# Kernel tuning notes

Measured on AMD Instinct MI355X. Metric: run time of the kernel, lower is better.

## Reference

```python
import jax, jax.numpy as jnp
import numpy as np
from jax import lax

EPS = 1e-5
B, T, I, H = 524288, 6, 4, 20


def batchnorm1d(x, gamma, beta):
    # x: [B, C, L]; training-mode BatchNorm1d over (batch, L) per channel C,
    # biased variance, matching torch's normalization in train().
    mean = jnp.mean(x, axis=(0, 2), keepdims=True)
    var = jnp.mean(jnp.square(x - mean), axis=(0, 2), keepdims=True)
    xhat = (x - mean) * lax.rsqrt(var + EPS)
    return xhat * gamma[None, :, None] + beta[None, :, None]


def lstm_layer(x, W_ih, W_hh, b_ih, b_hh):
    # x: [B, T, in]; torch gate order i, f, g, o; returns h sequence [B, T, H]
    Bsz = x.shape[0]
    Hd = W_hh.shape[1]
    # precompute input contribution for all steps: [B, T, 4H]
    xg = jnp.einsum('bti,gi->btg', x, W_ih) + b_ih + b_hh

    def step(carry, xg_t):
        h, c = carry
        g = xg_t + h @ W_hh.T  # [B, 4H]
        i, f, gg, o = jnp.split(g, 4, axis=-1)
        i = jax.nn.sigmoid(i)
        f = jax.nn.sigmoid(f)
        gg = jnp.tanh(gg)
        o = jax.nn.sigmoid(o)
        c = f * c + i * gg
        h = o * jnp.tanh(c)
        return (h, c), h

    h0 = jnp.zeros((Bsz, Hd), x.dtype)
    c0 = jnp.zeros((Bsz, Hd), x.dtype)
    _, hs = lax.scan(step, (h0, c0), jnp.swapaxes(xg, 0, 1))  # [T, B, H]
    return jnp.swapaxes(hs, 0, 1)


def setup_inputs() -> dict:
    key = jax.random.key(0)
    ks = jax.random.split(key, 12)
    s_ih0 = 1.0 / np.sqrt(H)
    d = {
        'x': jax.random.normal(ks[0], (B, T, I), jnp.float32),
        'gamma': jnp.ones((T,), jnp.float32),
        'beta': jnp.zeros((T,), jnp.float32),
        'W_ih0': jax.random.uniform(ks[1], (4 * H, I), jnp.float32, -s_ih0, s_ih0),
        'W_hh0': jax.random.uniform(ks[2], (4 * H, H), jnp.float32, -s_ih0, s_ih0),
        'b_ih0': jax.random.uniform(ks[3], (4 * H,), jnp.float32, -s_ih0, s_ih0),
        'b_hh0': jax.random.uniform(ks[4], (4 * H,), jnp.float32, -s_ih0, s_ih0),
        'W_ih1': jax.random.uniform(ks[5], (4 * H, H), jnp.float32, -s_ih0, s_ih0),
        'W_hh1': jax.random.uniform(ks[6], (4 * H, H), jnp.float32, -s_ih0, s_ih0),
        'b_ih1': jax.random.uniform(ks[7], (4 * H,), jnp.float32, -s_ih0, s_ih0),
        'b_hh1': jax.random.uniform(ks[8], (4 * H,), jnp.float32, -s_ih0, s_ih0),
        'W_out': jax.random.uniform(ks[9], (1, H), jnp.float32, -s_ih0, s_ih0),
        'b_out': jax.random.uniform(ks[10], (1,), jnp.float32, -s_ih0, s_ih0),
    }
    return d


def reference(x, gamma, beta, W_ih0, W_hh0, b_ih0, b_hh0,
              W_ih1, W_hh1, b_ih1, b_hh1, W_out, b_out):
    # bn over time-channel axis (C = TIME_STEP = 6)
    x = batchnorm1d(x, gamma, beta)                # [B, 6, 4]
    h1 = lstm_layer(x, W_ih0, W_hh0, b_ih0, b_hh0)  # [B, 6, 20]
    h2 = lstm_layer(h1, W_ih1, W_hh1, b_ih1, b_hh1)  # [B, 6, 20]
    r = batchnorm1d(h2, gamma, beta)               # same shared bn module
    out = r[:, -1, :] @ W_out.T + b_out            # [B, 1]
    return out
```

## Files before the change

kernel.cpp:

```cpp
#include <hip/hip_runtime.h>

#define EPS 1e-5f
#define BATCH 524288
#define BLK 256
#define RBLK 256
#define NBLK2 4096
#define NBLKO 2048

typedef float f32x4 __attribute__((ext_vector_type(4)));
typedef __bf16 bf16x8 __attribute__((ext_vector_type(8)));
typedef __bf16 bf16x4 __attribute__((ext_vector_type(4)));

#define AF_A0    0
#define AF_A1K0  5120
#define AF_A1K1  10240
#define AF_TOT   11520
#define OFF_BIAS0 5760
#define OFF_BIAS1 5840
#define OFF_ST    5920
#define OFF_P1    5936
#define OFF_P2    (OFF_P1 + RBLK * 12)

__device__ __forceinline__ float sigm(float x) {
    return __builtin_amdgcn_rcpf(1.0f + __expf(-x));
}
__device__ __forceinline__ float tanh_f(float x) {
    return 1.0f - 2.0f * __builtin_amdgcn_rcpf(1.0f + __expf(2.0f * x));
}
__device__ __forceinline__ float wave_reduce(float v) {
    #pragma unroll
    for (int o = 32; o; o >>= 1) v += __shfl_down(v, o, 64);
    return v;
}

struct HiLo { bf16x8 hi, lo; };
__device__ __forceinline__ HiLo cvt8(f32x4 a, f32x4 b) {
    HiLo r;
    #pragma unroll
    for (int i = 0; i < 4; ++i) {
        float v = a[i];
        __bf16 h = (__bf16)v;
        r.hi[i] = h; r.lo[i] = (__bf16)(v - (float)h);
        float w = b[i];
        __bf16 h2 = (__bf16)w;
        r.hi[4 + i] = h2; r.lo[4 + i] = (__bf16)(w - (float)h2);
    }
    return r;
}
__device__ __forceinline__ bf16x8 zb8() {
    bf16x8 z;
    #pragma unroll
    for (int i = 0; i < 8; ++i) z[i] = (__bf16)0.f;
    return z;
}
#define MFMA16(C_, A_, B_) \
    (C_) = __builtin_amdgcn_mfma_f32_16x16x32_bf16((A_), (B_), (C_), 0, 0, 0)

__global__ __launch_bounds__(BLK) void k_prep(
    const float* __restrict__ Wih0, const float* __restrict__ Whh0,
    const float* __restrict__ bih0, const float* __restrict__ bhh0,
    const float* __restrict__ Wih1, const float* __restrict__ Whh1,
    const float* __restrict__ bih1, const float* __restrict__ bhh1,
    float* __restrict__ ws) {
    const int tid = threadIdx.x;
    unsigned short* af = (unsigned short*)ws;
    for (int idx = tid; idx < AF_TOT; idx += BLK) {
        float w; int s;
        if (idx < AF_A1K0) {
            int e = idx, fid = e >> 9; e &= 511;
            int l = e >> 3, i = e & 7;
            int tm = fid >> 1; s = fid & 1;
            int q = l >> 4, m = l & 15;
            int wrow = (m & 3) * 20 + 4 * tm + (m >> 2);
            int k = 4 * q + (i & 3) + 16 * (i >> 2);
            w = (k < 20) ? Whh0[wrow * 20 + k]
              : (k < 24) ? Wih0[wrow * 4 + (k - 20)] : 0.f;
        } else if (idx < AF_A1K1) {
            int e = idx - AF_A1K0, fid = e >> 9; e &= 511;
            int l = e >> 3, i = e & 7;
            int tm = fid >> 1; s = fid & 1;
            int q = l >> 4, m = l & 15;
            int wrow = (m & 3) * 20 + 4 * tm + (m >> 2);
            int k = 4 * q + (i & 3) + 16 * (i >> 2);
            w = (k < 20) ? Wih1[wrow * 20 + k] : Whh1[wrow * 20 + (k - 20)];
        } else {
            int e = idx - AF_A1K1, fid = e >> 7; e &= 127;
            int l = e >> 2, i = e & 3;
            int tm = fid >> 1; s = fid & 1;
            int q = l >> 4, m = l & 15;
            int wrow = (m & 3) * 20 + 4 * tm + (m >> 2);
            int wcol = 12 + 4 * q + i;
            w = Whh1[wrow * 20 + wcol];
        }
        float fh = (float)(__bf16)w;
        float v = s ? (w - fh) : w;
        __bf16 bv = (__bf16)v;
        af[idx] = __builtin_bit_cast(unsigned short, bv);
    }
    for (int j = tid; j < 80; j += BLK) {
        int tm = j >> 4, q = (j >> 2) & 3, g = j & 3;
        int wrow = g * 20 + 4 * tm + q;
        ws[OFF_BIAS0 + j] = bih0[wrow] + bhh0[wrow];
        ws[OFF_BIAS1 + j] = bih1[wrow] + bhh1[wrow];
    }
}

__global__ __launch_bounds__(BLK) void k_reduce_x(const float* __restrict__ x,
                                                  float* __restrict__ part1) {
    float s[6], q[6];
    #pragma unroll
    for (int t = 0; t < 6; ++t) { s[t] = 0.f; q[t] = 0.f; }
    for (int b = blockIdx.x * BLK + threadIdx.x; b < BATCH; b += RBLK * BLK) {
        const float4* xp = (const float4*)(x + (size_t)b * 24);
        #pragma unroll
        for (int t = 0; t < 6; ++t) {
            float4 v = xp[t];
            s[t] += (v.x + v.y) + (v.z + v.w);
            q[t] += (v.x * v.x + v.y * v.y) + (v.z * v.z + v.w * v.w);
        }
    }
    __shared__ float red[4 * 12];
    int wid = threadIdx.x >> 6, lane = threadIdx.x & 63;
    #pragma unroll
    for (int c = 0; c < 6; ++c) {
        float rs = wave_reduce(s[c]);
        float rq = wave_reduce(q[c]);
        if (lane == 0) { red[wid * 12 + c] = rs; red[wid * 12 + 6 + c] = rq; }
    }
    __syncthreads();
    if (threadIdx.x < 12) {
        float tot = red[threadIdx.x] + red[12 + threadIdx.x] +
                    red[24 + threadIdx.x] + red[36 + threadIdx.x];
        part1[blockIdx.x * 12 + threadIdx.x] = tot;
    }
}

__global__ __launch_bounds__(BLK) void k_stats1(const float* __restrict__ part1,
                                                const float* __restrict__ gamma,
                                                const float* __restrict__ beta,
                                                float* __restrict__ stats) {
    float acc[12];
    #pragma unroll
    for (int c = 0; c < 12; ++c) acc[c] = 0.f;
    for (int p = threadIdx.x; p < RBLK; p += BLK) {
        #pragma unroll
        for (int c = 0; c < 12; ++c) acc[c] += part1[p * 12 + c];
    }
    __shared__ float red[4 * 12];
    __shared__ float tot[12];
    int wid = threadIdx.x >> 6, lane = threadIdx.x & 63;
    #pragma unroll
    for (int c = 0; c < 12; ++c) {
        float r = wave_reduce(acc[c]);
        if (lane == 0) red[wid * 12 + c] = r;
    }
    __syncthreads();
    if (threadIdx.x < 12) {
        tot[threadIdx.x] = red[threadIdx.x] + red[12 + threadIdx.x] +
                           red[24 + threadIdx.x] + red[36 + threadIdx.x];
    }
    __syncthreads();
    if (threadIdx.x < 6) {
        int t = threadIdx.x;
        const float N = (float)BATCH * 4.0f;
        float mean = tot[t] / N;
        float var = tot[6 + t] / N - mean * mean;
        float inv = rsqrtf(var + EPS);
        float a = gamma[t] * inv;
        stats[t] = a;
        stats[6 + t] = beta[t] - mean * a;
    }
}

__global__ __launch_bounds__(BLK, 3) void k_lstm(
    const float* __restrict__ x,
    const float* __restrict__ wsT,
    const float* __restrict__ Wout,
    const float* __restrict__ stats,
    float* __restrict__ dotout, float* __restrict__ part2) {
    __shared__ __align__(16) unsigned short sAF[AF_TOT];
    __shared__ __align__(16) float sBias[160];
    __shared__ __align__(16) float sBounce[4 * 1408];

    const int tid = threadIdx.x;
    {
        const unsigned int* src = (const unsigned int*)wsT;
        unsigned int* dst = (unsigned int*)sAF;
        for (int m = tid; m < AF_TOT / 2; m += BLK) dst[m] = src[m];
        for (int m = tid; m < 160; m += BLK) sBias[m] = wsT[OFF_BIAS0 + m];
    }
    float sA[12];
    #pragma unroll
    for (int c = 0; c < 12; ++c) sA[c] = stats[c];

    const int wid = tid >> 6, lane = tid & 63;
    const int q = lane >> 4, col = lane & 15;
    const int wb = blockIdx.x * 128 + wid * 32;
    float* buf = sBounce + wid * 1408;
    float* bc0 = buf + col * 44;
    float* bc1 = bc0 + 16 * 44;

    __syncthreads();
    for (int m = lane; m < 1408; m += 64) buf[m] = 0.f;

    float c0s[5][2], c1s[5][2], h1v[5][2];
    #pragma unroll
    for (int tm = 0; tm < 5; ++tm)
        #pragma unroll
        for (int nt = 0; nt < 2; ++nt) { c0s[tm][nt] = 0.f; c1s[tm][nt] = 0.f; h1v[tm][nt] = 0.f; }

    const float* xb0 = x + (size_t)(wb + col) * 24 + q;
    const float* xb1 = x + (size_t)(wb + 16 + col) * 24 + q;

    #pragma unroll 1
    for (int t = 0; t < 6; ++t) {
        int zo = 0;
        asm volatile("" : "+s"(zo));
        const unsigned short* AF = sAF + zo;
        const float* BI = sBias + zo;

        float at = sA[t], bt = sA[6 + t];
        bc0[40 + q] = fmaf(at, xb0[t * 4], bt);
        bc1[40 + q] = fmaf(at, xb1[t * 4], bt);

        HiLo b0[2];
        #pragma unroll
        for (int nt = 0; nt < 2; ++nt) {
            const float* bp = nt ? bc1 : bc0;
            f32x4 va = *(const f32x4*)(bp + 4 * q);
            f32x4 vb = {0.f, 0.f, 0.f, 0.f};
            if (q < 2) vb = *(const f32x4*)(bp + (q ? 40 : 16));
            b0[nt] = cvt8(va, vb);
        }
        #pragma unroll
        for (int tm = 0; tm < 5; ++tm) {
            f32x4 bias = *(const f32x4*)(BI + tm * 16 + q * 4);
            bf16x8 ahi = *(const bf16x8*)(AF + AF_A0 + (2 * tm) * 512 + lane * 8);
            bf16x8 alo = *(const bf16x8*)(AF + AF_A0 + (2 * tm + 1) * 512 + lane * 8);
            #pragma unroll
            for (int nt = 0; nt < 2; ++nt) {
                f32x4 c = bias;
                MFMA16(c, ahi, b0[nt].hi);
                MFMA16(c, ahi, b0[nt].lo);
                MFMA16(c, alo, b0[nt].hi);
                float ii = sigm(c[0]), ff = sigm(c[1]);
                float gg = tanh_f(c[2]), oo = sigm(c[3]);
                float cn = fmaf(ff, c0s[tm][nt], ii * gg);
                c0s[tm][nt] = cn;
                float h = oo * tanh_f(cn);
                (nt ? bc1 : bc0)[4 * tm + q] = h;
            }
        }

        HiLo b1[2], b2[2];
        #pragma unroll
        for (int nt = 0; nt < 2; ++nt) {
            const float* bp = nt ? bc1 : bc0;
            f32x4 va = *(const f32x4*)(bp + 4 * q);
            f32x4 vb = *(const f32x4*)(bp + 16 + 4 * q);
            b1[nt] = cvt8(va, vb);
            f32x4 vc = {0.f, 0.f, 0.f, 0.f};
            if (q < 2) vc = *(const f32x4*)(bp + 32 + 4 * q);
            f32x4 vz = {0.f, 0.f, 0.f, 0.f};
            b2[nt] = cvt8(vc, vz);
        }
        #pragma unroll
        for (int tm = 0; tm < 5; ++tm) {
            f32x4 bias = *(const f32x4*)(BI + 80 + tm * 16 + q * 4);
            bf16x8 ahi0 = *(const bf16x8*)(AF + AF_A1K0 + (2 * tm) * 512 + lane * 8);
            bf16x8 alo0 = *(const bf16x8*)(AF + AF_A1K0 + (2 * tm + 1) * 512 + lane * 8);
            bf16x8 ahi1 = zb8(), alo1 = zb8();
            if (q < 2) {
                bf16x4 th = *(const bf16x4*)(AF + AF_A1K1 + (2 * tm) * 128 + lane * 4);
                bf16x4 tl = *(const bf16x4*)(AF + AF_A1K1 + (2 * tm + 1) * 128 + lane * 4);
                #pragma unroll
                for (int i = 0; i < 4; ++i) { ahi1[i] = th[i]; alo1[i] = tl[i]; }
            }
            #pragma unroll
            for (int nt = 0; nt < 2; ++nt) {
                f32x4 c = bias;
                MFMA16(c, ahi0, b1[nt].hi);
                MFMA16(c, ahi0, b1[nt].lo);
                MFMA16(c, alo0, b1[nt].hi);
                MFMA16(c, ahi1, b2[nt].hi);
                MFMA16(c, ahi1, b2[nt].lo);
                MFMA16(c, alo1, b2[nt].hi);
                float ii = sigm(c[0]), ff = sigm(c[1]);
                float gg = tanh_f(c[2]), oo = sigm(c[3]);
                float cn = fmaf(ff, c1s[tm][nt], ii * gg);
                c1s[tm][nt] = cn;
                float h = oo * tanh_f(cn);
                h1v[tm][nt] = h;
                (nt ? bc1 : bc0)[20 + 4 * tm + q] = h;
            }
        }
    }

    float wout[5];
    #pragma unroll
    for (int tm = 0; tm < 5; ++tm) wout[tm] = Wout[4 * tm + q];
    float psum = 0.f, psq = 0.f;
    float dsum[2];
    #pragma unroll
    for (int nt = 0; nt < 2; ++nt) {
        float d = 0.f;
        #pragma unroll
        for (int tm = 0; tm < 5; ++tm) {
            float v = h1v[tm][nt];
            d = fmaf(v, wout[tm], d);
            psum += v; psq = fmaf(v, v, psq);
        }
        d += __shfl_xor(d, 16);
        d += __shfl_xor(d, 32);
        dsum[nt] = d;
    }
    if (q == 0) {
        dotout[wb + col] = dsum[0];
        dotout[wb + 16 + col] = dsum[1];
    }
    psum = wave_reduce(psum);
    psq = wave_reduce(psq);
    __syncthreads();
    if (lane == 0) { sBounce[wid] = psum; sBounce[4 + wid] = psq; }
    __syncthreads();
    if (tid == 0) {
        part2[blockIdx.x * 2 + 0] = sBounce[0] + sBounce[1] + sBounce[2] + sBounce[3];
        part2[blockIdx.x * 2 + 1] = sBounce[4] + sBounce[5] + sBounce[6] + sBounce[7];
    }
}

__global__ __launch_bounds__(BLK) void k_stats2(const float* __restrict__ part2,
                                                const float* __restrict__ gamma,
                                                const float* __restrict__ beta,
                                                const float* __restrict__ Wout,
                                                const float* __restrict__ bout,
                                                float* __restrict__ stats) {
    float s = 0.f, q = 0.f;
    for (int p = threadIdx.x; p < NBLK2; p += BLK) {
        s += part2[2 * p]; q += part2[2 * p + 1];
    }
    __shared__ float red[8];
    s = wave_reduce(s);
    q = wave_reduce(q);
    int wid = threadIdx.x >> 6, lane = threadIdx.x & 63;
    if (lane == 0) { red[wid] = s; red[4 + wid] = q; }
    __syncthreads();
    if (threadIdx.x == 0) {
        float S = red[0] + red[1] + red[2] + red[3];
        float Q = red[4] + red[5] + red[6] + red[7];
        const float N = (float)BATCH * 20.0f;
        float m = S / N, var = Q / N - m * m;
        float inv = rsqrtf(var + EPS);
        float s1 = gamma[5] * inv;
        float sw = 0.f;
        for (int h = 0; h < 20; ++h) sw += Wout[h];
        stats[12] = s1;
        stats[13] = (beta[5] - m * s1) * sw + bout[0];
    }
}

__global__ __launch_bounds__(BLK) void k_out(float* __restrict__ out,
                                             const float* __restrict__ stats) {
    int i = blockIdx.x * BLK + threadIdx.x;
    out[i] = stats[12] * out[i] + stats[13];
}

extern "C" void kernel_launch(void* const* d_in, const int* in_sizes, int n_in,
                              void* d_out, int out_size, void* d_ws, size_t ws_size,
                              hipStream_t stream) {
    const float* x     = (const float*)d_in[0];
    const float* gamma = (const float*)d_in[1];
    const float* beta  = (const float*)d_in[2];
    const float* Wih0  = (const float*)d_in[3];
    const float* Whh0  = (const float*)d_in[4];
    const float* bih0  = (const float*)d_in[5];
    const float* bhh0  = (const float*)d_in[6];
    const float* Wih1  = (const float*)d_in[7];
    const float* Whh1  = (const float*)d_in[8];
    const float* bih1  = (const float*)d_in[9];
    const float* bhh1  = (const float*)d_in[10];
    const float* Wout  = (const float*)d_in[11];
    const float* bout  = (const float*)d_in[12];
    float* out = (float*)d_out;
    float* ws = (float*)d_ws;

    float* part1 = ws + OFF_P1;
    float* part2 = ws + OFF_P2;
    float* stats = ws + OFF_ST;

    k_prep<<<1, BLK, 0, stream>>>(Wih0, Whh0, bih0, bhh0,
                                  Wih1, Whh1, bih1, bhh1, ws);
    k_reduce_x<<<RBLK, BLK, 0, stream>>>(x, part1);
    k_stats1<<<1, BLK, 0, stream>>>(part1, gamma, beta, stats);
    k_lstm<<<NBLK2, BLK, 0, stream>>>(x, ws, Wout, stats, out, part2);
    k_stats2<<<1, BLK, 0, stream>>>(part2, gamma, beta, Wout, bout, stats);
    k_out<<<NBLKO, BLK, 0, stream>>>(out, stats);
}
```

Before: 331.6 us.

## Fold biases into MFMA weights, keep weights in registers, replace stats kernels with atomics

Removes the two single-block stats kernels by accumulating batch statistics with global atomicAdd and recomputing mean/var inline in the LSTM and output kernels. Biases are folded into the MFMA weight fragments via a constant-1 input column, and the weight fragments are loaded once into registers instead of being staged in shared memory. The prep kernel is spread across 60 blocks, the x reduction uses more blocks, and the next x value is prefetched. The changes cut launches and LDS traffic but raise register pressure (launch bounds 1) and make the reductions order-nondeterministic.

```diff
diff --git a/kernel.cpp b/kernel.cpp
--- a/kernel.cpp
+++ b/kernel.cpp
@@ -3,23 +3,19 @@
 #define EPS 1e-5f
 #define BATCH 524288
 #define BLK 256
-#define RBLK 256
+#define RBLK 1024
+#define NPREP 60
 #define NBLK2 4096
 #define NBLKO 2048
 
 typedef float f32x4 __attribute__((ext_vector_type(4)));
 typedef __bf16 bf16x8 __attribute__((ext_vector_type(8)));
-typedef __bf16 bf16x4 __attribute__((ext_vector_type(4)));
 
 #define AF_A0    0
 #define AF_A1K0  5120
 #define AF_A1K1  10240
-#define AF_TOT   11520
-#define OFF_BIAS0 5760
-#define OFF_BIAS1 5840
-#define OFF_ST    5920
-#define OFF_P1    5936
-#define OFF_P2    (OFF_P1 + RBLK * 12)
+#define AF_TOT   15360
+#define OFF_ACC  7680
 
 __device__ __forceinline__ float sigm(float x) {
     return __builtin_amdgcn_rcpf(1.0f + __expf(-x));
@@ -47,12 +43,6 @@
     }
     return r;
 }
-__device__ __forceinline__ bf16x8 zb8() {
-    bf16x8 z;
-    #pragma unroll
-    for (int i = 0; i < 8; ++i) z[i] = (__bf16)0.f;
-    return z;
-}
 #define MFMA16(C_, A_, B_) \
     (C_) = __builtin_amdgcn_mfma_f32_16x16x32_bf16((A_), (B_), (C_), 0, 0, 0)
 
@@ -62,10 +52,11 @@
     const float* __restrict__ Wih1, const float* __restrict__ Whh1,
     const float* __restrict__ bih1, const float* __restrict__ bhh1,
     float* __restrict__ ws) {
-    const int tid = threadIdx.x;
+    int gtid = blockIdx.x * BLK + threadIdx.x;
     unsigned short* af = (unsigned short*)ws;
-    for (int idx = tid; idx < AF_TOT; idx += BLK) {
-        float w; int s;
+    if (gtid < AF_TOT) {
+        int idx = gtid;
+        float w = 0.f; int s;
         if (idx < AF_A1K0) {
             int e = idx, fid = e >> 9; e &= 511;
             int l = e >> 3, i = e & 7;
@@ -74,7 +65,8 @@
             int wrow = (m & 3) * 20 + 4 * tm + (m >> 2);
             int k = 4 * q + (i & 3) + 16 * (i >> 2);
             w = (k < 20) ? Whh0[wrow * 20 + k]
-              : (k < 24) ? Wih0[wrow * 4 + (k - 20)] : 0.f;
+              : (k < 24) ? Wih0[wrow * 4 + (k - 20)]
+              : (k == 24) ? (bih0[wrow] + bhh0[wrow]) : 0.f;
         } else if (idx < AF_A1K1) {
             int e = idx - AF_A1K0, fid = e >> 9; e &= 511;
             int l = e >> 3, i = e & 7;
@@ -84,29 +76,23 @@
             int k = 4 * q + (i & 3) + 16 * (i >> 2);
             w = (k < 20) ? Wih1[wrow * 20 + k] : Whh1[wrow * 20 + (k - 20)];
         } else {
-            int e = idx - AF_A1K1, fid = e >> 7; e &= 127;
-            int l = e >> 2, i = e & 3;
+            int e = idx - AF_A1K1, fid = e >> 9; e &= 511;
+            int l = e >> 3, i = e & 7;
             int tm = fid >> 1; s = fid & 1;
             int q = l >> 4, m = l & 15;
             int wrow = (m & 3) * 20 + 4 * tm + (m >> 2);
-            int wcol = 12 + 4 * q + i;
-            w = Whh1[wrow * 20 + wcol];
+            w = (q < 2 && i < 4) ? Whh1[wrow * 20 + 12 + 4 * q + i]
+              : (q == 2 && i == 0) ? (bih1[wrow] + bhh1[wrow]) : 0.f;
         }
         float fh = (float)(__bf16)w;
         float v = s ? (w - fh) : w;
-        __bf16 bv = (__bf16)v;
-        af[idx] = __builtin_bit_cast(unsigned short, bv);
-    }
-    for (int j = tid; j < 80; j += BLK) {
-        int tm = j >> 4, q = (j >> 2) & 3, g = j & 3;
-        int wrow = g * 20 + 4 * tm + q;
-        ws[OFF_BIAS0 + j] = bih0[wrow] + bhh0[wrow];
-        ws[OFF_BIAS1 + j] = bih1[wrow] + bhh1[wrow];
-    }
+        af[idx] = __builtin_bit_cast(unsigned short, (__bf16)v);
+    }
+    if (gtid < 16) ws[OFF_ACC + gtid] = 0.f;
 }
 
 __global__ __launch_bounds__(BLK) void k_reduce_x(const float* __restrict__ x,
-                                                  float* __restrict__ part1) {
+                                                  float* __restrict__ acc) {
     float s[6], q[6];
     #pragma unroll
     for (int t = 0; t < 6; ++t) { s[t] = 0.f; q[t] = 0.f; }
@@ -131,68 +117,19 @@
     if (threadIdx.x < 12) {
         float tot = red[threadIdx.x] + red[12 + threadIdx.x] +
                     red[24 + threadIdx.x] + red[36 + threadIdx.x];
-        part1[blockIdx.x * 12 + threadIdx.x] = tot;
-    }
-}
-
-__global__ __launch_bounds__(BLK) void k_stats1(const float* __restrict__ part1,
-                                                const float* __restrict__ gamma,
-                                                const float* __restrict__ beta,
-                                                float* __restrict__ stats) {
-    float acc[12];
-    #pragma unroll
-    for (int c = 0; c < 12; ++c) acc[c] = 0.f;
-    for (int p = threadIdx.x; p < RBLK; p += BLK) {
-        #pragma unroll
-        for (int c = 0; c < 12; ++c) acc[c] += part1[p * 12 + c];
-    }
-    __shared__ float red[4 * 12];
-    __shared__ float tot[12];
-    int wid = threadIdx.x >> 6, lane = threadIdx.x & 63;
-    #pragma unroll
-    for (int c = 0; c < 12; ++c) {
-        float r = wave_reduce(acc[c]);
-        if (lane == 0) red[wid * 12 + c] = r;
-    }
-    __syncthreads();
-    if (threadIdx.x < 12) {
-        tot[threadIdx.x] = red[threadIdx.x] + red[12 + threadIdx.x] +
-                           red[24 + threadIdx.x] + red[36 + threadIdx.x];
-    }
-    __syncthreads();
-    if (threadIdx.x < 6) {
-        int t = threadIdx.x;
-        const float N = (float)BATCH * 4.0f;
-        float mean = tot[t] / N;
-        float var = tot[6 + t] / N - mean * mean;
-        float inv = rsqrtf(var + EPS);
-        float a = gamma[t] * inv;
-        stats[t] = a;
-        stats[6 + t] = beta[t] - mean * a;
-    }
-}
-
-__global__ __launch_bounds__(BLK, 3) void k_lstm(
+        atomicAdd(&acc[threadIdx.x], tot);
+    }
+}
+
+__global__ __launch_bounds__(BLK, 1) void k_lstm(
     const float* __restrict__ x,
     const float* __restrict__ wsT,
+    const float* __restrict__ gamma, const float* __restrict__ beta,
     const float* __restrict__ Wout,
-    const float* __restrict__ stats,
-    float* __restrict__ dotout, float* __restrict__ part2) {
-    __shared__ __align__(16) unsigned short sAF[AF_TOT];
-    __shared__ __align__(16) float sBias[160];
+    float* __restrict__ dotout, float* __restrict__ acc2) {
     __shared__ __align__(16) float sBounce[4 * 1408];
 
     const int tid = threadIdx.x;
-    {
-        const unsigned int* src = (const unsigned int*)wsT;
-        unsigned int* dst = (unsigned int*)sAF;
-        for (int m = tid; m < AF_TOT / 2; m += BLK) dst[m] = src[m];
-        for (int m = tid; m < 160; m += BLK) sBias[m] = wsT[OFF_BIAS0 + m];
-    }
-    float sA[12];
-    #pragma unroll
-    for (int c = 0; c < 12; ++c) sA[c] = stats[c];
-
     const int wid = tid >> 6, lane = tid & 63;
     const int q = lane >> 4, col = lane & 15;
     const int wb = blockIdx.x * 128 + wid * 32;
@@ -200,28 +137,44 @@
     float* bc0 = buf + col * 44;
     float* bc1 = bc0 + 16 * 44;
 
-    __syncthreads();
+    const unsigned short* af = (const unsigned short*)wsT;
+    bf16x8 A0h[5], A0l[5], A1h[5], A1l[5], A2h[5], A2l[5];
+    #pragma unroll
+    for (int tm = 0; tm < 5; ++tm) {
+        A0h[tm] = *(const bf16x8*)(af + AF_A0   + (2 * tm) * 512 + lane * 8);
+        A0l[tm] = *(const bf16x8*)(af + AF_A0   + (2 * tm + 1) * 512 + lane * 8);
+        A1h[tm] = *(const bf16x8*)(af + AF_A1K0 + (2 * tm) * 512 + lane * 8);
+        A1l[tm] = *(const bf16x8*)(af + AF_A1K0 + (2 * tm + 1) * 512 + lane * 8);
+        A2h[tm] = *(const bf16x8*)(af + AF_A1K1 + (2 * tm) * 512 + lane * 8);
+        A2l[tm] = *(const bf16x8*)(af + AF_A1K1 + (2 * tm + 1) * 512 + lane * 8);
+    }
+    const float* accp = wsT + OFF_ACC;
+
     for (int m = lane; m < 1408; m += 64) buf[m] = 0.f;
 
-    float c0s[5][2], c1s[5][2], h1v[5][2];
+    float c0s[5][2], c1s[5][2];
     #pragma unroll
     for (int tm = 0; tm < 5; ++tm)
         #pragma unroll
-        for (int nt = 0; nt < 2; ++nt) { c0s[tm][nt] = 0.f; c1s[tm][nt] = 0.f; h1v[tm][nt] = 0.f; }
+        for (int nt = 0; nt < 2; ++nt) { c0s[tm][nt] = 0.f; c1s[tm][nt] = 0.f; }
 
     const float* xb0 = x + (size_t)(wb + col) * 24 + q;
     const float* xb1 = x + (size_t)(wb + 16 + col) * 24 + q;
+    float x0c = xb0[0], x1c = xb1[0];
 
     #pragma unroll 1
     for (int t = 0; t < 6; ++t) {
-        int zo = 0;
-        asm volatile("" : "+s"(zo));
-        const unsigned short* AF = sAF + zo;
-        const float* BI = sBias + zo;
-
-        float at = sA[t], bt = sA[6 + t];
-        bc0[40 + q] = fmaf(at, xb0[t * 4], bt);
-        bc1[40 + q] = fmaf(at, xb1[t * 4], bt);
+        const float invN = 1.0f / ((float)BATCH * 4.0f);
+        float mean = accp[t] * invN;
+        float var = accp[6 + t] * invN - mean * mean;
+        float inv = rsqrtf(var + EPS);
+        float at = gamma[t] * inv;
+        float bt = beta[t] - mean * at;
+
+        float x0n = 0.f, x1n = 0.f;
+        if (t < 5) { x0n = xb0[(t + 1) * 4]; x1n = xb1[(t + 1) * 4]; }
+        bc0[40 + q] = fmaf(at, x0c, bt);
+        bc1[40 + q] = fmaf(at, x1c, bt);
 
         HiLo b0[2];
         #pragma unroll
@@ -230,25 +183,22 @@
             f32x4 va = *(const f32x4*)(bp + 4 * q);
             f32x4 vb = {0.f, 0.f, 0.f, 0.f};
             if (q < 2) vb = *(const f32x4*)(bp + (q ? 40 : 16));
+            else if (q == 2) vb[0] = 1.0f;
             b0[nt] = cvt8(va, vb);
         }
         #pragma unroll
         for (int tm = 0; tm < 5; ++tm) {
-            f32x4 bias = *(const f32x4*)(BI + tm * 16 + q * 4);
-            bf16x8 ahi = *(const bf16x8*)(AF + AF_A0 + (2 * tm) * 512 + lane * 8);
-            bf16x8 alo = *(const bf16x8*)(AF + AF_A0 + (2 * tm + 1) * 512 + lane * 8);
             #pragma unroll
             for (int nt = 0; nt < 2; ++nt) {
-                f32x4 c = bias;
-                MFMA16(c, ahi, b0[nt].hi);
-                MFMA16(c, ahi, b0[nt].lo);
-                MFMA16(c, alo, b0[nt].hi);
+                f32x4 c = {0.f, 0.f, 0.f, 0.f};
+                MFMA16(c, A0h[tm], b0[nt].hi);
+                MFMA16(c, A0h[tm], b0[nt].lo);
+                MFMA16(c, A0l[tm], b0[nt].hi);
                 float ii = sigm(c[0]), ff = sigm(c[1]);
                 float gg = tanh_f(c[2]), oo = sigm(c[3]);
                 float cn = fmaf(ff, c0s[tm][nt], ii * gg);
                 c0s[tm][nt] = cn;
-                float h = oo * tanh_f(cn);
-                (nt ? bc1 : bc0)[4 * tm + q] = h;
+                (nt ? bc1 : bc0)[4 * tm + q] = oo * tanh_f(cn);
             }
         }
 
@@ -261,39 +211,29 @@
             b1[nt] = cvt8(va, vb);
             f32x4 vc = {0.f, 0.f, 0.f, 0.f};
             if (q < 2) vc = *(const f32x4*)(bp + 32 + 4 * q);
+            else if (q == 2) vc[0] = 1.0f;
             f32x4 vz = {0.f, 0.f, 0.f, 0.f};
             b2[nt] = cvt8(vc, vz);
         }
         #pragma unroll
         for (int tm = 0; tm < 5; ++tm) {
-            f32x4 bias = *(const f32x4*)(BI + 80 + tm * 16 + q * 4);
-            bf16x8 ahi0 = *(const bf16x8*)(AF + AF_A1K0 + (2 * tm) * 512 + lane * 8);
-            bf16x8 alo0 = *(const bf16x8*)(AF + AF_A1K0 + (2 * tm + 1) * 512 + lane * 8);
-            bf16x8 ahi1 = zb8(), alo1 = zb8();
-            if (q < 2) {
-                bf16x4 th = *(const bf16x4*)(AF + AF_A1K1 + (2 * tm) * 128 + lane * 4);
-                bf16x4 tl = *(const bf16x4*)(AF + AF_A1K1 + (2 * tm + 1) * 128 + lane * 4);
-                #pragma unroll
-                for (int i = 0; i < 4; ++i) { ahi1[i] = th[i]; alo1[i] = tl[i]; }
-            }
             #pragma unroll
             for (int nt = 0; nt < 2; ++nt) {
-                f32x4 c = bias;
-                MFMA16(c, ahi0, b1[nt].hi);
-                MFMA16(c, ahi0, b1[nt].lo);
-                MFMA16(c, alo0, b1[nt].hi);
-                MFMA16(c, ahi1, b2[nt].hi);
-                MFMA16(c, ahi1, b2[nt].lo);
-                MFMA16(c, alo1, b2[nt].hi);
+                f32x4 c = {0.f, 0.f, 0.f, 0.f};
+                MFMA16(c, A1h[tm], b1[nt].hi);
+                MFMA16(c, A1h[tm], b1[nt].lo);
+                MFMA16(c, A1l[tm], b1[nt].hi);
+                MFMA16(c, A2h[tm], b2[nt].hi);
+                MFMA16(c, A2h[tm], b2[nt].lo);
+                MFMA16(c, A2l[tm], b2[nt].hi);
                 float ii = sigm(c[0]), ff = sigm(c[1]);
                 float gg = tanh_f(c[2]), oo = sigm(c[3]);
                 float cn = fmaf(ff, c1s[tm][nt], ii * gg);
                 c1s[tm][nt] = cn;
-                float h = oo * tanh_f(cn);
-                h1v[tm][nt] = h;
-                (nt ? bc1 : bc0)[20 + 4 * tm + q] = h;
+                (nt ? bc1 : bc0)[20 + 4 * tm + q] = oo * tanh_f(cn);
             }
         }
+        x0c = x0n; x1c = x1n;
     }
 
     float wout[5];
@@ -303,10 +243,11 @@
     float dsum[2];
     #pragma unroll
     for (int nt = 0; nt < 2; ++nt) {
+        const float* bp = nt ? bc1 : bc0;
         float d = 0.f;
         #pragma unroll
         for (int tm = 0; tm < 5; ++tm) {
-            float v = h1v[tm][nt];
+            float v = bp[20 + 4 * tm + q];
             d = fmaf(v, wout[tm], d);
             psum += v; psq = fmaf(v, v, psq);
         }
@@ -324,45 +265,27 @@
     if (lane == 0) { sBounce[wid] = psum; sBounce[4 + wid] = psq; }
     __syncthreads();
     if (tid == 0) {
-        part2[blockIdx.x * 2 + 0] = sBounce[0] + sBounce[1] + sBounce[2] + sBounce[3];
-        part2[blockIdx.x * 2 + 1] = sBounce[4] + sBounce[5] + sBounce[6] + sBounce[7];
-    }
-}
-
-__global__ __launch_bounds__(BLK) void k_stats2(const float* __restrict__ part2,
-                                                const float* __restrict__ gamma,
-                                                const float* __restrict__ beta,
-                                                const float* __restrict__ Wout,
-                                                const float* __restrict__ bout,
-                                                float* __restrict__ stats) {
-    float s = 0.f, q = 0.f;
-    for (int p = threadIdx.x; p < NBLK2; p += BLK) {
-        s += part2[2 * p]; q += part2[2 * p + 1];
-    }
-    __shared__ float red[8];
-    s = wave_reduce(s);
-    q = wave_reduce(q);
-    int wid = threadIdx.x >> 6, lane = threadIdx.x & 63;
-    if (lane == 0) { red[wid] = s; red[4 + wid] = q; }
-    __syncthreads();
-    if (threadIdx.x == 0) {
-        float S = red[0] + red[1] + red[2] + red[3];
-        float Q = red[4] + red[5] + red[6] + red[7];
-        const float N = (float)BATCH * 20.0f;
-        float m = S / N, var = Q / N - m * m;
-        float inv = rsqrtf(var + EPS);
-        float s1 = gamma[5] * inv;
-        float sw = 0.f;
-        for (int h = 0; h < 20; ++h) sw += Wout[h];
-        stats[12] = s1;
-        stats[13] = (beta[5] - m * s1) * sw + bout[0];
+        atomicAdd(&acc2[0], sBounce[0] + sBounce[1] + sBounce[2] + sBounce[3]);
+        atomicAdd(&acc2[1], sBounce[4] + sBounce[5] + sBounce[6] + sBounce[7]);
     }
 }
 
 __global__ __launch_bounds__(BLK) void k_out(float* __restrict__ out,
-                                             const float* __restrict__ stats) {
+                                             const float* __restrict__ ws,
+                                             const float* __restrict__ gamma,
+                                             const float* __restrict__ beta,
+                                             const float* __restrict__ Wout,
+                                             const float* __restrict__ bout) {
+    float S = ws[OFF_ACC + 12], Q = ws[OFF_ACC + 13];
+    const float N = (float)BATCH * 20.0f;
+    float m = S / N, var = Q / N - m * m;
+    float s1 = gamma[5] * rsqrtf(var + EPS);
+    float sw = 0.f;
+    #pragma unroll
+    for (int h = 0; h < 20; ++h) sw += Wout[h];
+    float s2 = (beta[5] - m * s1) * sw + bout[0];
     int i = blockIdx.x * BLK + threadIdx.x;
-    out[i] = stats[12] * out[i] + stats[13];
+    out[i] = s1 * out[i] + s2;
 }
 
 extern "C" void kernel_launch(void* const* d_in, const int* in_sizes, int n_in,
@@ -384,15 +307,10 @@
     float* out = (float*)d_out;
     float* ws = (float*)d_ws;
 
-    float* part1 = ws + OFF_P1;
-    float* part2 = ws + OFF_P2;
-    float* stats = ws + OFF_ST;
-
-    k_prep<<<1, BLK, 0, stream>>>(Wih0, Whh0, bih0, bhh0,
-                                  Wih1, Whh1, bih1, bhh1, ws);
-    k_reduce_x<<<RBLK, BLK, 0, stream>>>(x, part1);
-    k_stats1<<<1, BLK, 0, stream>>>(part1, gamma, beta, stats);
-    k_lstm<<<NBLK2, BLK, 0, stream>>>(x, ws, Wout, stats, out, part2);
-    k_stats2<<<1, BLK, 0, stream>>>(part2, gamma, beta, Wout, bout, stats);
-    k_out<<<NBLKO, BLK, 0, stream>>>(out, stats);
-}
+    k_prep<<<NPREP, BLK, 0, stream>>>(Wih0, Whh0, bih0, bhh0,
+                                      Wih1, Whh1, bih1, bhh1, ws);
+    k_reduce_x<<<RBLK, BLK, 0, stream>>>(x, ws + OFF_ACC);
+    k_lstm<<<NBLK2, BLK, 0, stream>>>(x, ws, gamma, beta, Wout,
+                                      out, ws + OFF_ACC + 12);
+    k_out<<<NBLKO, BLK, 0, stream>>>(out, ws, gamma, beta, Wout, bout);
+}
```

Result: no change. 334.3 us (+0.8%).
